# Kernel optimization log

Hardware: AMD Instinct MI355X
Metric: run time of the kernel (lower is better)

## Reference

```python
import jax, jax.numpy as jnp
import numpy as np

EPS = 1e-5

def layer_norm(x, g, b):
    mu = jnp.mean(x, axis=-1, keepdims=True)
    var = jnp.var(x, axis=-1, keepdims=True)
    return (x - mu) * jax.lax.rsqrt(var + EPS) * g + b

def setup_inputs() -> dict:
    key = jax.random.key(0)
    ks = jax.random.split(key, 16)
    N, E, D, ED = 50000, 500000, 128, 5
    def w(k, i, o):
        return jax.random.normal(k, (i, o), jnp.float32) / np.sqrt(i)
    return {
        "x": jax.random.normal(ks[0], (N, D), jnp.float32),
        "edge_attr": jax.random.normal(ks[1], (E, ED), jnp.float32),
        "pos": jax.random.normal(ks[2], (N, 3), jnp.float32),
        "node_w1": w(ks[3], D, D), "node_b1": jnp.zeros((D,), jnp.float32),
        "node_g1": jnp.ones((D,), jnp.float32), "node_be1": jnp.zeros((D,), jnp.float32),
        "node_w2": w(ks[4], D, D), "node_b2": jnp.zeros((D,), jnp.float32),
        "edge_w1": w(ks[5], 2 * D + ED, D), "edge_b1": jnp.zeros((D,), jnp.float32),
        "edge_g1": jnp.ones((D,), jnp.float32), "edge_be1": jnp.zeros((D,), jnp.float32),
        "edge_w2": w(ks[6], D, D), "edge_b2": jnp.zeros((D,), jnp.float32),
        "upd_w": w(ks[7], 2 * D, D), "upd_b": jnp.zeros((D,), jnp.float32),
        "ln_g": jnp.ones((D,), jnp.float32), "ln_b": jnp.zeros((D,), jnp.float32),
        "edge_index": jax.random.randint(ks[8], (2, E), 0, N, jnp.int64),
    }

def reference(x, edge_attr, pos, node_w1, node_b1, node_g1, node_be1, node_w2, node_b2,
              edge_w1, edge_b1, edge_g1, edge_be1, edge_w2, edge_b2,
              upd_w, upd_b, ln_g, ln_b, edge_index):
    N = x.shape[0]
    # node MLP: Linear -> LayerNorm -> ReLU -> Linear (dropout=0)
    h_nodes = jax.nn.relu(layer_norm(x @ node_w1 + node_b1, node_g1, node_be1)) @ node_w2 + node_b2
    src, dst = edge_index[0], edge_index[1]
    # edge MLP on gathered endpoint features + edge_attr  [E, 2D+edge_dim]
    ef = jnp.concatenate([x[src], x[dst], edge_attr], axis=1)
    h_edges = jax.nn.relu(layer_norm(ef @ edge_w1 + edge_b1, edge_g1, edge_be1)) @ edge_w2 + edge_b2
    # scatter-add aggregation to destination nodes
    h_agg = jax.ops.segment_sum(h_edges, dst, num_segments=N)
    h_out = jnp.concatenate([h_nodes, h_agg], axis=1) @ upd_w + upd_b
    h_out = h_out + x  # residual (in_channels == out_channels)
    return layer_norm(h_out, ln_g, ln_b)
```

## Files before the change

kernel.cpp:

```cpp
#include <hip/hip_runtime.h>
#include <stdint.h>

#define D    128
#define ED   5
#define BLK  512
#define WPB  8
#define W1S  296
#define W2S  136
#define HS   136
#define US   264
#define GRID 256

typedef __attribute__((ext_vector_type(8))) short bf16x8;
typedef __attribute__((ext_vector_type(4))) float f32x4;

__device__ __forceinline__ unsigned short f2bf(float f) {
    union { float f; uint32_t u; } c; c.f = f;
    uint32_t r = (c.u + 0x7fffu + ((c.u >> 16) & 1u)) >> 16;
    return (unsigned short)r;
}
__device__ __forceinline__ float bflo(uint32_t u) {
    union { uint32_t u; float f; } c; c.u = u << 16; return c.f;
}
__device__ __forceinline__ float bfhi(uint32_t u) {
    union { uint32_t u; float f; } c; c.u = u & 0xffff0000u; return c.f;
}
__device__ __forceinline__ bf16x8 cvt8(const float* __restrict__ p) {
    float4 a = *(const float4*)p;
    float4 b = *(const float4*)(p + 4);
    bf16x8 r;
    r[0] = (short)f2bf(a.x); r[1] = (short)f2bf(a.y);
    r[2] = (short)f2bf(a.z); r[3] = (short)f2bf(a.w);
    r[4] = (short)f2bf(b.x); r[5] = (short)f2bf(b.y);
    r[6] = (short)f2bf(b.z); r[7] = (short)f2bf(b.w);
    return r;
}
__device__ __forceinline__ bool detect64(const int* ei) {
    return (ei[1] == 0) & (ei[3] == 0) & (ei[5] == 0) &
           (ei[7] == 0) & (ei[9] == 0) & (ei[11] == 0);
}

__global__ __launch_bounds__(512)
void cvt_count_kernel(const float* __restrict__ in, unsigned short* __restrict__ out,
                      int n8, const int* __restrict__ ei, int* __restrict__ cnt, int E) {
    const int i = blockIdx.x * 512 + threadIdx.x;
    if (i < n8) {
        float4 a = ((const float4*)in)[2 * i];
        float4 b = ((const float4*)in)[2 * i + 1];
        union { unsigned short s[8]; uint4 v; } p;
        p.s[0] = f2bf(a.x); p.s[1] = f2bf(a.y); p.s[2] = f2bf(a.z); p.s[3] = f2bf(a.w);
        p.s[4] = f2bf(b.x); p.s[5] = f2bf(b.y); p.s[6] = f2bf(b.z); p.s[7] = f2bf(b.w);
        ((uint4*)out)[i] = p.v;
    } else {
        const int e = i - n8;
        if (e < E) {
            const bool is64 = detect64(ei);
            int d = is64 ? ei[2 * ((size_t)E + e)] : ei[(size_t)E + e];
            atomicAdd(&cnt[d], 1);
        }
    }
}

__global__ __launch_bounds__(1024)
void scan_blk_kernel(const int* __restrict__ cnt, int* __restrict__ part,
                     int* __restrict__ bsum, int N) {
    __shared__ int wsum[16];
    const int tid = threadIdx.x, wave = tid >> 6, lane = tid & 63;
    const int idx = blockIdx.x * 1024 + tid;
    int v = (idx < N) ? cnt[idx] : 0;
    int s = v;
    #pragma unroll
    for (int off = 1; off < 64; off <<= 1) {
        int t = __shfl_up(s, off, 64);
        if (lane >= off) s += t;
    }
    if (lane == 63) wsum[wave] = s;
    __syncthreads();
    if (wave == 0 && lane < 16) {
        int ws_ = wsum[lane];
        #pragma unroll
        for (int off = 1; off < 16; off <<= 1) {
            int t = __shfl_up(ws_, off, 64);
            if (lane >= off) ws_ += t;
        }
        wsum[lane] = ws_;
    }
    __syncthreads();
    const int excl = ((wave == 0) ? 0 : wsum[wave - 1]) + (s - v);
    if (idx < N) part[idx] = excl;
    if (tid == 0) bsum[blockIdx.x] = wsum[15];
}

__global__ __launch_bounds__(1024)
void scan_top_kernel(int* __restrict__ bsum, int nb) {
    __shared__ int wsum[16];
    const int tid = threadIdx.x, wave = tid >> 6, lane = tid & 63;
    int v = (tid < nb) ? bsum[tid] : 0;
    int s = v;
    #pragma unroll
    for (int off = 1; off < 64; off <<= 1) {
        int t = __shfl_up(s, off, 64);
        if (lane >= off) s += t;
    }
    if (lane == 63) wsum[wave] = s;
    __syncthreads();
    if (wave == 0 && lane < 16) {
        int ws_ = wsum[lane];
        #pragma unroll
        for (int off = 1; off < 16; off <<= 1) {
            int t = __shfl_up(ws_, off, 64);
            if (lane >= off) ws_ += t;
        }
        wsum[lane] = ws_;
    }
    __syncthreads();
    const int excl = ((wave == 0) ? 0 : wsum[wave - 1]) + (s - v);
    if (tid < nb) bsum[tid] = excl;
}

__global__ __launch_bounds__(1024)
void scan_add_kernel(const int* __restrict__ part, const int* __restrict__ bsum,
                     int* __restrict__ starts, int* __restrict__ cursor,
                     int N, int E) {
    const int idx = blockIdx.x * 1024 + threadIdx.x;
    if (idx < N) {
        int v = part[idx] + bsum[blockIdx.x];
        starts[idx] = v;
        cursor[idx] = v;
    }
    if (blockIdx.x == 0 && threadIdx.x == 0) starts[N] = E;
}

__global__ __launch_bounds__(512)
void fill_kernel(const int* __restrict__ ei, int* __restrict__ cursor,
                 int* __restrict__ slotp, int E) {
    const bool is64 = detect64(ei);
    int e = blockIdx.x * 512 + threadIdx.x;
    if (e >= E) return;
    int d = is64 ? ei[2 * ((size_t)E + e)] : ei[(size_t)E + e];
    slotp[e] = atomicAdd(&cursor[d], 1);
}

template<bool EDGE, bool XBF, bool CSR>
__global__ __launch_bounds__(BLK, 2)
void mlp_kernel(const float* __restrict__ x, const unsigned short* __restrict__ xbf,
                const float* __restrict__ ea, const int* __restrict__ ei,
                const int* __restrict__ slotp,
                const float* __restrict__ w1, const float* __restrict__ b1,
                const float* __restrict__ g1, const float* __restrict__ be1,
                const float* __restrict__ w2, const float* __restrict__ b2,
                unsigned short* __restrict__ hout, float* __restrict__ aggf,
                int N, int E)
{
    __shared__ unsigned short w1t[128 * W1S];
    __shared__ unsigned short w2t[128 * W2S];
    __shared__ unsigned short hb[WPB][16 * HS];

    const int tid = threadIdx.x;
    const int KROWS = EDGE ? 288 : 128;
    for (int i = tid; i < KROWS * 128; i += BLK) {
        int k = i >> 7, n = i & 127;
        float v = (!EDGE || k < (2 * D + ED)) ? w1[k * 128 + n] : 0.f;
        w1t[n * W1S + k] = f2bf(v);
    }
    for (int i = tid; i < 128 * 128; i += BLK) {
        int k = i >> 7, n = i & 127;
        w2t[n * W2S + k] = f2bf(w2[k * 128 + n]);
    }
    __syncthreads();

    bool is64 = false;
    if (EDGE) is64 = detect64(ei);

    const int lane = tid & 63, w = tid >> 6;
    const int g = lane >> 4, c = lane & 15;

    float b1v[8], g1v[8], e1v[8], b2v[8];
    #pragma unroll
    for (int nt = 0; nt < 8; ++nt) {
        b1v[nt] = b1[nt * 16 + c];  g1v[nt] = g1[nt * 16 + c];
        e1v[nt] = be1[nt * 16 + c]; b2v[nt] = b2[nt * 16 + c];
    }

    const int cnt = EDGE ? E : N;
    const int nT = (cnt + 15) >> 4;
    const int step = gridDim.x * WPB;
    unsigned short* hw = hb[w];

    int pdd = 0, prc = 0, psl = 0;
    size_t paoff = 0, pboff = 0;
    bf16x8 pf[9];

    auto loadIdx = [&](int tl) {
        const int rr = tl * 16 + c;
        const int rc = rr < cnt ? rr : cnt - 1;
        prc = rc;
        if (EDGE) {
            int s = is64 ? ei[2 * (size_t)rc]       : ei[rc];
            pdd   = is64 ? ei[2 * ((size_t)E + rc)] : ei[(size_t)E + rc];
            paoff = (size_t)s * D;
            pboff = (size_t)pdd * D;
            if (CSR) psl = slotp[rc];
        } else {
            paoff = (size_t)rc * D;
        }
    };
    auto loadFrags = [&]() {
        #pragma unroll
        for (int kk = 0; kk < (EDGE ? 8 : 4); ++kk) {
            const size_t o = (kk < 4) ? paoff + kk * 32 : pboff + (kk - 4) * 32;
            if (XBF) pf[kk] = *(const bf16x8*)(xbf + o + 8 * g);
            else     pf[kk] = cvt8(x + o + 8 * g);
        }
        if (EDGE) {
            bf16x8 t;
            #pragma unroll
            for (int j = 0; j < 8; ++j) t[j] = 0;
            if (g == 0) {
                #pragma unroll
                for (int j = 0; j < ED; ++j)
                    t[j] = (short)f2bf(ea[(size_t)prc * ED + j]);
            }
            pf[8] = t;
        }
    };

    int tile = blockIdx.x * WPB + w;
    if (tile < nT) { loadIdx(tile); loadFrags(); }

    for (; tile < nT; tile += step) {
        bf16x8 af[9];
        #pragma unroll
        for (int kk = 0; kk < (EDGE ? 9 : 4); ++kk) af[kk] = pf[kk];
        const int dd = pdd;
        const int sl = psl;
        const int row = tile * 16 + c;

        const int tn = tile + step;
        loadIdx(tn < nT ? tn : tile);

        const f32x4 z = {0.f, 0.f, 0.f, 0.f};
        f32x4 acc[8] = {z, z, z, z, z, z, z, z};
        #pragma unroll
        for (int kk = 0; kk < (EDGE ? 9 : 4); ++kk) {
            const unsigned short* wr = &w1t[c * W1S + kk * 32 + 8 * g];
            #pragma unroll
            for (int nt = 0; nt < 8; ++nt) {
                bf16x8 bf = *(const bf16x8*)(wr + nt * 16 * W1S);
                acc[nt] = __builtin_amdgcn_mfma_f32_16x16x32_bf16(af[kk], bf, acc[nt], 0, 0, 0);
            }
        }

        loadFrags();

        float mean[4], rstd[4];
        #pragma unroll
        for (int r = 0; r < 4; ++r) {
            float s = 0.f, q = 0.f;
            #pragma unroll
            for (int nt = 0; nt < 8; ++nt) {
                float v = acc[nt][r] + b1v[nt];
                acc[nt][r] = v;
                s += v; q += v * v;
            }
            s += __shfl_xor(s, 1, 64); q += __shfl_xor(q, 1, 64);
            s += __shfl_xor(s, 2, 64); q += __shfl_xor(q, 2, 64);
            s += __shfl_xor(s, 4, 64); q += __shfl_xor(q, 4, 64);
            s += __shfl_xor(s, 8, 64); q += __shfl_xor(q, 8, 64);
            float m = s * (1.f / 128.f);
            float var = q * (1.f / 128.f) - m * m;
            mean[r] = m;
            rstd[r] = rsqrtf(var + 1e-5f);
        }
        #pragma unroll
        for (int nt = 0; nt < 8; ++nt) {
            #pragma unroll
            for (int r = 0; r < 4; ++r) {
                float h = fmaxf((acc[nt][r] - mean[r]) * rstd[r] * g1v[nt] + e1v[nt], 0.f);
                hw[(4 * g + r) * HS + nt * 16 + c] = f2bf(h);
            }
        }

        f32x4 acc2[8] = {z, z, z, z, z, z, z, z};
        #pragma unroll
        for (int kk = 0; kk < 4; ++kk) {
            bf16x8 hf = *(const bf16x8*)&hw[c * HS + kk * 32 + 8 * g];
            const unsigned short* wr = &w2t[c * W2S + kk * 32 + 8 * g];
            #pragma unroll
            for (int nt = 0; nt < 8; ++nt) {
                bf16x8 bf = *(const bf16x8*)(wr + nt * 16 * W2S);
                acc2[nt] = __builtin_amdgcn_mfma_f32_16x16x32_bf16(hf, bf, acc2[nt], 0, 0, 0);
            }
        }

        if (EDGE && !CSR) {
            int dv[4];
            #pragma unroll
            for (int r = 0; r < 4; ++r) dv[r] = __shfl(dd, 4 * g + r, 64);
            #pragma unroll
            for (int r = 0; r < 4; ++r) {
                const int er = tile * 16 + 4 * g + r;
                if (er < cnt) {
                    float* dst = aggf + (size_t)dv[r] * D + c;
                    #pragma unroll
                    for (int nt = 0; nt < 8; ++nt)
                        atomicAdd(dst + nt * 16, acc2[nt][r] + b2v[nt]);
                }
            }
        } else {
            #pragma unroll
            for (int nt = 0; nt < 8; ++nt) {
                #pragma unroll
                for (int r = 0; r < 4; ++r)
                    hw[(4 * g + r) * HS + nt * 16 + c] = f2bf(acc2[nt][r] + b2v[nt]);
            }
            if (row < cnt) {
                const int orow = (EDGE && CSR) ? sl : row;
                unsigned short* dst = hout + (size_t)orow * D;
                #pragma unroll
                for (int j = 0; j < 4; ++j)
                    *(uint4*)(dst + (j * 4 + g) * 8) =
                        *(const uint4*)&hw[c * HS + (j * 4 + g) * 8];
            }
        }
    }
}

template<bool XBF>
__global__ __launch_bounds__(BLK, 2)
void upd3_kernel(const unsigned short* __restrict__ hnb,
                 const unsigned short* __restrict__ h2, const int* __restrict__ starts,
                 const float* __restrict__ x, const unsigned short* __restrict__ xbf,
                 const float* __restrict__ uw, const float* __restrict__ ub,
                 const float* __restrict__ lg, const float* __restrict__ lb,
                 float* __restrict__ out, int N)
{
    __shared__ unsigned short wt[128 * US];
    const int tid = threadIdx.x;
    for (int i = tid; i < 256 * 128; i += BLK) {
        int k = i >> 7, n = i & 127;
        wt[n * US + k] = f2bf(uw[i]);
    }
    __syncthreads();

    const int lane = tid & 63, w = tid >> 6;
    const int g = lane >> 4, c = lane & 15;

    float ubv[8], gv[8], bv[8];
    #pragma unroll
    for (int nt = 0; nt < 8; ++nt) {
        ubv[nt] = ub[nt * 16 + c]; gv[nt] = lg[nt * 16 + c]; bv[nt] = lb[nt * 16 + c];
    }

    const int nT = (N + 15) >> 4;
    for (int tile = blockIdx.x * WPB + w; tile < nT; tile += gridDim.x * WPB) {
        const int row = tile * 16 + c;
        const int rc  = row < N ? row : N - 1;

        const int s = starts[rc], t = starts[rc + 1];
        float ag0[8] = {0,0,0,0,0,0,0,0}, ag1[8] = {0,0,0,0,0,0,0,0};
        float ag2[8] = {0,0,0,0,0,0,0,0}, ag3[8] = {0,0,0,0,0,0,0,0};
        for (int j = s; j < t; ++j) {
            const unsigned short* pr = h2 + (size_t)j * D + 8 * g;
            uint4 v0 = *(const uint4*)(pr);
            uint4 v1 = *(const uint4*)(pr + 32);
            uint4 v2 = *(const uint4*)(pr + 64);
            uint4 v3 = *(const uint4*)(pr + 96);
            ag0[0] += bflo(v0.x); ag0[1] += bfhi(v0.x); ag0[2] += bflo(v0.y); ag0[3] += bfhi(v0.y);
            ag0[4] += bflo(v0.z); ag0[5] += bfhi(v0.z); ag0[6] += bflo(v0.w); ag0[7] += bfhi(v0.w);
            ag1[0] += bflo(v1.x); ag1[1] += bfhi(v1.x); ag1[2] += bflo(v1.y); ag1[3] += bfhi(v1.y);
            ag1[4] += bflo(v1.z); ag1[5] += bfhi(v1.z); ag1[6] += bflo(v1.w); ag1[7] += bfhi(v1.w);
            ag2[0] += bflo(v2.x); ag2[1] += bfhi(v2.x); ag2[2] += bflo(v2.y); ag2[3] += bfhi(v2.y);
            ag2[4] += bflo(v2.z); ag2[5] += bfhi(v2.z); ag2[6] += bflo(v2.w); ag2[7] += bfhi(v2.w);
            ag3[0] += bflo(v3.x); ag3[1] += bfhi(v3.x); ag3[2] += bflo(v3.y); ag3[3] += bfhi(v3.y);
            ag3[4] += bflo(v3.z); ag3[5] += bfhi(v3.z); ag3[6] += bflo(v3.w); ag3[7] += bfhi(v3.w);
        }

        const f32x4 z = {0.f, 0.f, 0.f, 0.f};
        f32x4 acc[8] = {z, z, z, z, z, z, z, z};

        #pragma unroll
        for (int kk = 0; kk < 8; ++kk) {
            bf16x8 af;
            if (kk < 4) {
                af = *(const bf16x8*)(hnb + (size_t)rc * D + kk * 32 + 8 * g);
            } else {
                const float* agp = (kk == 4) ? ag0 : (kk == 5) ? ag1 : (kk == 6) ? ag2 : ag3;
                #pragma unroll
                for (int i = 0; i < 8; ++i) af[i] = (short)f2bf(agp[i]);
            }
            const unsigned short* wr = &wt[c * US + kk * 32 + 8 * g];
            #pragma unroll
            for (int nt = 0; nt < 8; ++nt) {
                bf16x8 bf = *(const bf16x8*)(wr + nt * 16 * US);
                acc[nt] = __builtin_amdgcn_mfma_f32_16x16x32_bf16(af, bf, acc[nt], 0, 0, 0);
            }
        }

        float mean[4], rstd[4];
        #pragma unroll
        for (int r = 0; r < 4; ++r) {
            const int row4 = tile * 16 + 4 * g + r;
            const int r4c = row4 < N ? row4 : N - 1;
            float s2 = 0.f, q = 0.f;
            #pragma unroll
            for (int nt = 0; nt < 8; ++nt) {
                float xr;
                if (XBF) xr = bflo((uint32_t)xbf[(size_t)r4c * D + nt * 16 + c]);
                else     xr = x[(size_t)r4c * D + nt * 16 + c];
                float v = acc[nt][r] + ubv[nt] + xr;
                acc[nt][r] = v;
                s2 += v; q += v * v;
            }
            s2 += __shfl_xor(s2, 1, 64); q += __shfl_xor(q, 1, 64);
            s2 += __shfl_xor(s2, 2, 64); q += __shfl_xor(q, 2, 64);
            s2 += __shfl_xor(s2, 4, 64); q += __shfl_xor(q, 4, 64);
            s2 += __shfl_xor(s2, 8, 64); q += __shfl_xor(q, 8, 64);
            float m = s2 * (1.f / 128.f);
            mean[r] = m;
            rstd[r] = rsqrtf(q * (1.f / 128.f) - m * m + 1e-5f);
        }
        #pragma unroll
        for (int r = 0; r < 4; ++r) {
            const int row4 = tile * 16 + 4 * g + r;
            if (row4 < N) {
                #pragma unroll
                for (int nt = 0; nt < 8; ++nt)
                    out[(size_t)row4 * D + nt * 16 + c] =
                        (acc[nt][r] - mean[r]) * rstd[r] * gv[nt] + bv[nt];
            }
        }
    }
}

template<bool AGGBF, bool XBF>
__global__ __launch_bounds__(BLK, 4)
void upd2_kernel(const unsigned short* __restrict__ hnb, const void* __restrict__ aggp,
                 const float* __restrict__ x, const unsigned short* __restrict__ xbf,
                 const float* __restrict__ uw, const float* __restrict__ ub,
                 const float* __restrict__ lg, const float* __restrict__ lb,
                 float* __restrict__ out, int N)
{
    __shared__ unsigned short wt[128 * US];
    const int tid = threadIdx.x;
    for (int i = tid; i < 256 * 128; i += BLK) {
        int k = i >> 7, n = i & 127;
        wt[n * US + k] = f2bf(uw[i]);
    }
    __syncthreads();

    const int lane = tid & 63, w = tid >> 6;
    const int g = lane >> 4, c = lane & 15;

    float ubv[8], gv[8], bv[8];
    #pragma unroll
    for (int nt = 0; nt < 8; ++nt) {
        ubv[nt] = ub[nt * 16 + c]; gv[nt] = lg[nt * 16 + c]; bv[nt] = lb[nt * 16 + c];
    }

    const int nT = (N + 15) >> 4;
    for (int tile = blockIdx.x * WPB + w; tile < nT; tile += gridDim.x * WPB) {
        const int row = tile * 16 + c;
        const int rc  = row < N ? row : N - 1;

        const f32x4 z = {0.f, 0.f, 0.f, 0.f};
        f32x4 acc[8] = {z, z, z, z, z, z, z, z};

        #pragma unroll
        for (int kk = 0; kk < 8; ++kk) {
            bf16x8 af;
            if (kk < 4) {
                af = *(const bf16x8*)(hnb + (size_t)rc * D + kk * 32 + 8 * g);
            } else {
                if (AGGBF)
                    af = *(const bf16x8*)((const unsigned short*)aggp +
                                          (size_t)rc * D + (kk - 4) * 32 + 8 * g);
                else
                    af = cvt8((const float*)aggp + (size_t)rc * D + (kk - 4) * 32 + 8 * g);
            }
            const unsigned short* wr = &wt[c * US + kk * 32 + 8 * g];
            #pragma unroll
            for (int nt = 0; nt < 8; ++nt) {
                bf16x8 bf = *(const bf16x8*)(wr + nt * 16 * US);
                acc[nt] = __builtin_amdgcn_mfma_f32_16x16x32_bf16(af, bf, acc[nt], 0, 0, 0);
            }
        }

        float mean[4], rstd[4];
        #pragma unroll
        for (int r = 0; r < 4; ++r) {
            const int row4 = tile * 16 + 4 * g + r;
            const int r4c = row4 < N ? row4 : N - 1;
            float s = 0.f, q = 0.f;
            #pragma unroll
            for (int nt = 0; nt < 8; ++nt) {
                float xr;
                if (XBF) xr = bflo((uint32_t)xbf[(size_t)r4c * D + nt * 16 + c]);
                else     xr = x[(size_t)r4c * D + nt * 16 + c];
                float v = acc[nt][r] + ubv[nt] + xr;
                acc[nt][r] = v;
                s += v; q += v * v;
            }
            s += __shfl_xor(s, 1, 64); q += __shfl_xor(q, 1, 64);
            s += __shfl_xor(s, 2, 64); q += __shfl_xor(q, 2, 64);
            s += __shfl_xor(s, 4, 64); q += __shfl_xor(q, 4, 64);
            s += __shfl_xor(s, 8, 64); q += __shfl_xor(q, 8, 64);
            float m = s * (1.f / 128.f);
            mean[r] = m;
            rstd[r] = rsqrtf(q * (1.f / 128.f) - m * m + 1e-5f);
        }
        #pragma unroll
        for (int r = 0; r < 4; ++r) {
            const int row4 = tile * 16 + 4 * g + r;
            if (row4 < N) {
                #pragma unroll
                for (int nt = 0; nt < 8; ++nt)
                    out[(size_t)row4 * D + nt * 16 + c] =
                        (acc[nt][r] - mean[r]) * rstd[r] * gv[nt] + bv[nt];
            }
        }
    }
}

extern "C" void kernel_launch(void* const* d_in, const int* in_sizes, int n_in,
                              void* d_out, int out_size, void* d_ws, size_t ws_size,
                              hipStream_t stream)
{
    const float* x    = (const float*)d_in[0];
    const float* ea   = (const float*)d_in[1];
    const float* nw1  = (const float*)d_in[3];
    const float* nb1  = (const float*)d_in[4];
    const float* ng1  = (const float*)d_in[5];
    const float* nbe1 = (const float*)d_in[6];
    const float* nw2  = (const float*)d_in[7];
    const float* nb2  = (const float*)d_in[8];
    const float* ew1  = (const float*)d_in[9];
    const float* eb1  = (const float*)d_in[10];
    const float* eg1  = (const float*)d_in[11];
    const float* ebe1 = (const float*)d_in[12];
    const float* ew2  = (const float*)d_in[13];
    const float* eb2  = (const float*)d_in[14];
    const float* uw   = (const float*)d_in[15];
    const float* ub   = (const float*)d_in[16];
    const float* lg   = (const float*)d_in[17];
    const float* lb   = (const float*)d_in[18];
    const int*   eidx = (const int*)d_in[19];

    const int N = in_sizes[0] / D;
    const int E = in_sizes[1] / ED;

    char* base = (char*)d_ws;
    size_t off = 0;
    auto alloc = [&](size_t bytes) -> char* {
        char* p = base + off;
        off = (off + bytes + 255) & ~(size_t)255;
        return p;
    };

    unsigned short* hnb  = (unsigned short*)alloc((size_t)N * D * 2);
    unsigned short* xbf  = (unsigned short*)alloc((size_t)N * D * 2);
    int* cnt    = (int*)alloc((size_t)N * 4);
    int* starts = (int*)alloc(((size_t)N + 1) * 4);
    int* cursor = (int*)alloc((size_t)N * 4);
    int* bsum   = (int*)alloc(1024 * 4);
    int* slotA  = (int*)alloc((size_t)E * 4);
    unsigned short* h2 = (unsigned short*)alloc((size_t)E * D * 2);
    const size_t needA = off;

    const int n8 = N * D / 8;
    const int egrid = (E + 511) / 512;
    const int nb = (N + 1023) / 1024;
    const int ugrid = (((N + 15) / 16) + WPB - 1) / WPB;

    if (ws_size >= needA && nb <= 1024) {
        hipMemsetAsync(cnt, 0, (size_t)N * 4, stream);
        cvt_count_kernel<<<(n8 + E + 511) / 512, 512, 0, stream>>>(
            x, xbf, n8, eidx, cnt, E);
        scan_blk_kernel<<<nb, 1024, 0, stream>>>(cnt, cursor, bsum, N);
        scan_top_kernel<<<1, 1024, 0, stream>>>(bsum, nb);
        scan_add_kernel<<<nb, 1024, 0, stream>>>(cursor, bsum, starts, cursor, N, E);
        fill_kernel<<<egrid, 512, 0, stream>>>(eidx, cursor, slotA, E);
        mlp_kernel<false, true, true><<<GRID, BLK, 0, stream>>>(
            x, xbf, nullptr, nullptr, nullptr, nw1, nb1, ng1, nbe1, nw2, nb2,
            hnb, nullptr, N, E);
        mlp_kernel<true, true, true><<<GRID, BLK, 0, stream>>>(
            x, xbf, ea, eidx, slotA, ew1, eb1, eg1, ebe1, ew2, eb2,
            h2, nullptr, N, E);
        upd3_kernel<true><<<ugrid, BLK, 0, stream>>>(
            hnb, h2, starts, x, xbf, uw, ub, lg, lb, (float*)d_out, N);
        return;
    }

    off = 0;
    unsigned short* hnb2 = (unsigned short*)alloc((size_t)N * D * 2);
    float* aggf = (float*)alloc((size_t)N * D * 4);
    unsigned short* xbf2 = (unsigned short*)alloc((size_t)N * D * 2);
    const size_t needB = off;

    hipMemsetAsync(aggf, 0, (size_t)N * D * 4, stream);
    if (ws_size >= needB) {
        cvt_count_kernel<<<(n8 + 511) / 512, 512, 0, stream>>>(
            x, xbf2, n8, nullptr, nullptr, 0);
        mlp_kernel<false, true, false><<<GRID, BLK, 0, stream>>>(
            x, xbf2, nullptr, nullptr, nullptr, nw1, nb1, ng1, nbe1, nw2, nb2,
            hnb2, nullptr, N, E);
        mlp_kernel<true, true, false><<<GRID, BLK, 0, stream>>>(
            x, xbf2, ea, eidx, nullptr, ew1, eb1, eg1, ebe1, ew2, eb2,
            nullptr, aggf, N, E);
        upd2_kernel<false, true><<<ugrid, BLK, 0, stream>>>(
            hnb2, aggf, x, xbf2, uw, ub, lg, lb, (float*)d_out, N);
    } else {
        mlp_kernel<false, false, false><<<GRID, BLK, 0, stream>>>(
            x, nullptr, nullptr, nullptr, nullptr, nw1, nb1, ng1, nbe1, nw2, nb2,
            hnb2, nullptr, N, E);
        mlp_kernel<true, false, false><<<GRID, BLK, 0, stream>>>(
            x, nullptr, ea, eidx, nullptr, ew1, eb1, eg1, ebe1, ew2, eb2,
            nullptr, aggf, N, E);
        upd2_kernel<false, false><<<ugrid, BLK, 0, stream>>>(
            hnb2, aggf, x, nullptr, uw, ub, lg, lb, (float*)d_out, N);
    }
}
```

Baseline: 410.0 us.

## Process two 16-edge tiles per wave in edge MLP and split node MLP kernel

The edge MLP now handles 32 edges per wave iteration. Each LDS weight fragment load feeds two MFMAs, one per 16-row tile, which halves weight-read traffic from shared memory per edge. The node MLP gets its own simpler kernel with a smaller w1 buffer. LDS stores of the hidden activations are packed into 32-bit pairs using lane shuffles. The fallback path is rewritten to use the CSR/upd3 approach, and the atomic and upd2 variants are removed. Doubling the prefetch and accumulator buffers raises register pressure under the 2-blocks-per-SM launch bound, which risks spills or lower occupancy.

```diff
diff --git a/kernel.cpp b/kernel.cpp
--- a/kernel.cpp
+++ b/kernel.cpp
@@ -141,26 +141,24 @@
     slotp[e] = atomicAdd(&cursor[d], 1);
 }
 
-template<bool EDGE, bool XBF, bool CSR>
+template<bool XBF>
 __global__ __launch_bounds__(BLK, 2)
-void mlp_kernel(const float* __restrict__ x, const unsigned short* __restrict__ xbf,
-                const float* __restrict__ ea, const int* __restrict__ ei,
-                const int* __restrict__ slotp,
-                const float* __restrict__ w1, const float* __restrict__ b1,
-                const float* __restrict__ g1, const float* __restrict__ be1,
-                const float* __restrict__ w2, const float* __restrict__ b2,
-                unsigned short* __restrict__ hout, float* __restrict__ aggf,
-                int N, int E)
+void edge_mlp(const float* __restrict__ x, const unsigned short* __restrict__ xbf,
+              const float* __restrict__ ea, const int* __restrict__ ei,
+              const int* __restrict__ slotp,
+              const float* __restrict__ w1, const float* __restrict__ b1,
+              const float* __restrict__ g1, const float* __restrict__ be1,
+              const float* __restrict__ w2, const float* __restrict__ b2,
+              unsigned short* __restrict__ h2, int E)
 {
     __shared__ unsigned short w1t[128 * W1S];
     __shared__ unsigned short w2t[128 * W2S];
     __shared__ unsigned short hb[WPB][16 * HS];
 
     const int tid = threadIdx.x;
-    const int KROWS = EDGE ? 288 : 128;
-    for (int i = tid; i < KROWS * 128; i += BLK) {
+    for (int i = tid; i < 288 * 128; i += BLK) {
         int k = i >> 7, n = i & 127;
-        float v = (!EDGE || k < (2 * D + ED)) ? w1[k * 128 + n] : 0.f;
+        float v = (k < (2 * D + ED)) ? w1[k * 128 + n] : 0.f;
         w1t[n * W1S + k] = f2bf(v);
     }
     for (int i = tid; i < 128 * 128; i += BLK) {
@@ -169,9 +167,7 @@
     }
     __syncthreads();
 
-    bool is64 = false;
-    if (EDGE) is64 = detect64(ei);
-
+    const bool is64 = detect64(ei);
     const int lane = tid & 63, w = tid >> 6;
     const int g = lane >> 4, c = lane & 15;
 
@@ -182,77 +178,57 @@
         e1v[nt] = be1[nt * 16 + c]; b2v[nt] = b2[nt * 16 + c];
     }
 
-    const int cnt = EDGE ? E : N;
-    const int nT = (cnt + 15) >> 4;
+    const int nT = (E + 31) >> 5;
     const int step = gridDim.x * WPB;
     unsigned short* hw = hb[w];
 
-    int pdd = 0, prc = 0, psl = 0;
-    size_t paoff = 0, pboff = 0;
-    bf16x8 pf[9];
+    int psl0 = 0, psl1 = 0, pe0 = 0, pe1 = 0;
+    size_t pa0 = 0, pb0 = 0, pa1 = 0, pb1 = 0;
+    bf16x8 pf0[9], pf1[9];
 
     auto loadIdx = [&](int tl) {
-        const int rr = tl * 16 + c;
-        const int rc = rr < cnt ? rr : cnt - 1;
-        prc = rc;
-        if (EDGE) {
-            int s = is64 ? ei[2 * (size_t)rc]       : ei[rc];
-            pdd   = is64 ? ei[2 * ((size_t)E + rc)] : ei[(size_t)E + rc];
-            paoff = (size_t)s * D;
-            pboff = (size_t)pdd * D;
-            if (CSR) psl = slotp[rc];
-        } else {
-            paoff = (size_t)rc * D;
-        }
+        const int r0 = tl * 32 + c;
+        const int r1 = tl * 32 + 16 + c;
+        const int rc0 = r0 < E ? r0 : E - 1;
+        const int rc1 = r1 < E ? r1 : E - 1;
+        pe0 = rc0; pe1 = rc1;
+        int s0 = is64 ? ei[2 * (size_t)rc0]       : ei[rc0];
+        int d0 = is64 ? ei[2 * ((size_t)E + rc0)] : ei[(size_t)E + rc0];
+        int s1 = is64 ? ei[2 * (size_t)rc1]       : ei[rc1];
+        int d1 = is64 ? ei[2 * ((size_t)E + rc1)] : ei[(size_t)E + rc1];
+        pa0 = (size_t)s0 * D; pb0 = (size_t)d0 * D;
+        pa1 = (size_t)s1 * D; pb1 = (size_t)d1 * D;
+        psl0 = slotp[rc0]; psl1 = slotp[rc1];
     };
     auto loadFrags = [&]() {
         #pragma unroll
-        for (int kk = 0; kk < (EDGE ? 8 : 4); ++kk) {
-            const size_t o = (kk < 4) ? paoff + kk * 32 : pboff + (kk - 4) * 32;
-            if (XBF) pf[kk] = *(const bf16x8*)(xbf + o + 8 * g);
-            else     pf[kk] = cvt8(x + o + 8 * g);
-        }
-        if (EDGE) {
-            bf16x8 t;
-            #pragma unroll
-            for (int j = 0; j < 8; ++j) t[j] = 0;
-            if (g == 0) {
-                #pragma unroll
-                for (int j = 0; j < ED; ++j)
-                    t[j] = (short)f2bf(ea[(size_t)prc * ED + j]);
-            }
-            pf[8] = t;
-        }
+        for (int kk = 0; kk < 8; ++kk) {
+            const size_t o0 = (kk < 4) ? pa0 + kk * 32 : pb0 + (kk - 4) * 32;
+            const size_t o1 = (kk < 4) ? pa1 + kk * 32 : pb1 + (kk - 4) * 32;
+            if (XBF) {
+                pf0[kk] = *(const bf16x8*)(xbf + o0 + 8 * g);
+                pf1[kk] = *(const bf16x8*)(xbf + o1 + 8 * g);
+            } else {
+                pf0[kk] = cvt8(x + o0 + 8 * g);
+                pf1[kk] = cvt8(x + o1 + 8 * g);
+            }
+        }
+        bf16x8 t0, t1;
+        #pragma unroll
+        for (int j = 0; j < 8; ++j) { t0[j] = 0; t1[j] = 0; }
+        if (g == 0) {
+            #pragma unroll
+            for (int j = 0; j < ED; ++j) {
+                t0[j] = (short)f2bf(ea[(size_t)pe0 * ED + j]);
+                t1[j] = (short)f2bf(ea[(size_t)pe1 * ED + j]);
+            }
+        }
+        pf0[8] = t0; pf1[8] = t1;
     };
 
-    int tile = blockIdx.x * WPB + w;
-    if (tile < nT) { loadIdx(tile); loadFrags(); }
-
-    for (; tile < nT; tile += step) {
-        bf16x8 af[9];
-        #pragma unroll
-        for (int kk = 0; kk < (EDGE ? 9 : 4); ++kk) af[kk] = pf[kk];
-        const int dd = pdd;
-        const int sl = psl;
-        const int row = tile * 16 + c;
-
-        const int tn = tile + step;
-        loadIdx(tn < nT ? tn : tile);
-
-        const f32x4 z = {0.f, 0.f, 0.f, 0.f};
-        f32x4 acc[8] = {z, z, z, z, z, z, z, z};
-        #pragma unroll
-        for (int kk = 0; kk < (EDGE ? 9 : 4); ++kk) {
-            const unsigned short* wr = &w1t[c * W1S + kk * 32 + 8 * g];
-            #pragma unroll
-            for (int nt = 0; nt < 8; ++nt) {
-                bf16x8 bf = *(const bf16x8*)(wr + nt * 16 * W1S);
-                acc[nt] = __builtin_amdgcn_mfma_f32_16x16x32_bf16(af[kk], bf, acc[nt], 0, 0, 0);
-            }
-        }
-
-        loadFrags();
-
+    const f32x4 z = {0.f, 0.f, 0.f, 0.f};
+
+    auto process = [&](f32x4* acc, int sl, int rowv) __attribute__((always_inline)) {
         float mean[4], rstd[4];
         #pragma unroll
         for (int r = 0; r < 4; ++r) {
@@ -268,19 +244,21 @@
             s += __shfl_xor(s, 4, 64); q += __shfl_xor(q, 4, 64);
             s += __shfl_xor(s, 8, 64); q += __shfl_xor(q, 8, 64);
             float m = s * (1.f / 128.f);
-            float var = q * (1.f / 128.f) - m * m;
             mean[r] = m;
-            rstd[r] = rsqrtf(var + 1e-5f);
+            rstd[r] = rsqrtf(q * (1.f / 128.f) - m * m + 1e-5f);
         }
         #pragma unroll
         for (int nt = 0; nt < 8; ++nt) {
             #pragma unroll
             for (int r = 0; r < 4; ++r) {
                 float h = fmaxf((acc[nt][r] - mean[r]) * rstd[r] * g1v[nt] + e1v[nt], 0.f);
-                hw[(4 * g + r) * HS + nt * 16 + c] = f2bf(h);
-            }
-        }
-
+                float hp = __shfl_xor(h, 1, 64);
+                if (!(c & 1)) {
+                    uint32_t pk = (uint32_t)f2bf(h) | ((uint32_t)f2bf(hp) << 16);
+                    *(uint32_t*)&hw[(4 * g + r) * HS + nt * 16 + c] = pk;
+                }
+            }
+        }
         f32x4 acc2[8] = {z, z, z, z, z, z, z, z};
         #pragma unroll
         for (int kk = 0; kk < 4; ++kk) {
@@ -292,36 +270,167 @@
                 acc2[nt] = __builtin_amdgcn_mfma_f32_16x16x32_bf16(hf, bf, acc2[nt], 0, 0, 0);
             }
         }
-
-        if (EDGE && !CSR) {
-            int dv[4];
-            #pragma unroll
-            for (int r = 0; r < 4; ++r) dv[r] = __shfl(dd, 4 * g + r, 64);
+        #pragma unroll
+        for (int nt = 0; nt < 8; ++nt) {
             #pragma unroll
             for (int r = 0; r < 4; ++r) {
-                const int er = tile * 16 + 4 * g + r;
-                if (er < cnt) {
-                    float* dst = aggf + (size_t)dv[r] * D + c;
-                    #pragma unroll
-                    for (int nt = 0; nt < 8; ++nt)
-                        atomicAdd(dst + nt * 16, acc2[nt][r] + b2v[nt]);
+                float o = acc2[nt][r] + b2v[nt];
+                float op = __shfl_xor(o, 1, 64);
+                if (!(c & 1)) {
+                    uint32_t pk = (uint32_t)f2bf(o) | ((uint32_t)f2bf(op) << 16);
+                    *(uint32_t*)&hw[(4 * g + r) * HS + nt * 16 + c] = pk;
                 }
             }
-        } else {
-            #pragma unroll
-            for (int nt = 0; nt < 8; ++nt) {
-                #pragma unroll
-                for (int r = 0; r < 4; ++r)
-                    hw[(4 * g + r) * HS + nt * 16 + c] = f2bf(acc2[nt][r] + b2v[nt]);
-            }
-            if (row < cnt) {
-                const int orow = (EDGE && CSR) ? sl : row;
-                unsigned short* dst = hout + (size_t)orow * D;
-                #pragma unroll
-                for (int j = 0; j < 4; ++j)
-                    *(uint4*)(dst + (j * 4 + g) * 8) =
-                        *(const uint4*)&hw[c * HS + (j * 4 + g) * 8];
-            }
+        }
+        if (rowv < E) {
+            unsigned short* dst = h2 + (size_t)sl * D;
+            #pragma unroll
+            for (int j = 0; j < 4; ++j)
+                *(uint4*)(dst + (j * 4 + g) * 8) =
+                    *(const uint4*)&hw[c * HS + (j * 4 + g) * 8];
+        }
+    };
+
+    int tile = blockIdx.x * WPB + w;
+    if (tile < nT) { loadIdx(tile); loadFrags(); }
+
+    for (; tile < nT; tile += step) {
+        f32x4 acc0[8] = {z, z, z, z, z, z, z, z};
+        f32x4 acc1[8] = {z, z, z, z, z, z, z, z};
+        #pragma unroll
+        for (int kk = 0; kk < 9; ++kk) {
+            const unsigned short* wr = &w1t[c * W1S + kk * 32 + 8 * g];
+            const bf16x8 a0 = pf0[kk], a1 = pf1[kk];
+            #pragma unroll
+            for (int nt = 0; nt < 8; ++nt) {
+                bf16x8 bf = *(const bf16x8*)(wr + nt * 16 * W1S);
+                acc0[nt] = __builtin_amdgcn_mfma_f32_16x16x32_bf16(a0, bf, acc0[nt], 0, 0, 0);
+                acc1[nt] = __builtin_amdgcn_mfma_f32_16x16x32_bf16(a1, bf, acc1[nt], 0, 0, 0);
+            }
+        }
+        const int sl0 = psl0, sl1 = psl1;
+        const int row0 = tile * 32 + c, row1 = tile * 32 + 16 + c;
+
+        const int tn = tile + step;
+        loadIdx(tn < nT ? tn : tile);
+        loadFrags();
+
+        process(acc0, sl0, row0);
+        process(acc1, sl1, row1);
+    }
+}
+
+template<bool XBF>
+__global__ __launch_bounds__(BLK, 2)
+void node_mlp(const float* __restrict__ x, const unsigned short* __restrict__ xbf,
+              const float* __restrict__ w1, const float* __restrict__ b1,
+              const float* __restrict__ g1, const float* __restrict__ be1,
+              const float* __restrict__ w2, const float* __restrict__ b2,
+              unsigned short* __restrict__ hnb, int N)
+{
+    __shared__ unsigned short w1t[128 * W2S];
+    __shared__ unsigned short w2t[128 * W2S];
+    __shared__ unsigned short hb[WPB][16 * HS];
+
+    const int tid = threadIdx.x;
+    for (int i = tid; i < 128 * 128; i += BLK) {
+        int k = i >> 7, n = i & 127;
+        w1t[n * W2S + k] = f2bf(w1[k * 128 + n]);
+        w2t[n * W2S + k] = f2bf(w2[k * 128 + n]);
+    }
+    __syncthreads();
+
+    const int lane = tid & 63, w = tid >> 6;
+    const int g = lane >> 4, c = lane & 15;
+
+    float b1v[8], g1v[8], e1v[8], b2v[8];
+    #pragma unroll
+    for (int nt = 0; nt < 8; ++nt) {
+        b1v[nt] = b1[nt * 16 + c];  g1v[nt] = g1[nt * 16 + c];
+        e1v[nt] = be1[nt * 16 + c]; b2v[nt] = b2[nt * 16 + c];
+    }
+
+    const int nT = (N + 15) >> 4;
+    const f32x4 z = {0.f, 0.f, 0.f, 0.f};
+    unsigned short* hw = hb[w];
+
+    for (int tile = blockIdx.x * WPB + w; tile < nT; tile += gridDim.x * WPB) {
+        const int row = tile * 16 + c;
+        const int rc  = row < N ? row : N - 1;
+
+        f32x4 acc[8] = {z, z, z, z, z, z, z, z};
+        #pragma unroll
+        for (int kk = 0; kk < 4; ++kk) {
+            bf16x8 af;
+            if (XBF) af = *(const bf16x8*)(xbf + (size_t)rc * D + kk * 32 + 8 * g);
+            else     af = cvt8(x + (size_t)rc * D + kk * 32 + 8 * g);
+            const unsigned short* wr = &w1t[c * W2S + kk * 32 + 8 * g];
+            #pragma unroll
+            for (int nt = 0; nt < 8; ++nt) {
+                bf16x8 bf = *(const bf16x8*)(wr + nt * 16 * W2S);
+                acc[nt] = __builtin_amdgcn_mfma_f32_16x16x32_bf16(af, bf, acc[nt], 0, 0, 0);
+            }
+        }
+
+        float mean[4], rstd[4];
+        #pragma unroll
+        for (int r = 0; r < 4; ++r) {
+            float s = 0.f, q = 0.f;
+            #pragma unroll
+            for (int nt = 0; nt < 8; ++nt) {
+                float v = acc[nt][r] + b1v[nt];
+                acc[nt][r] = v;
+                s += v; q += v * v;
+            }
+            s += __shfl_xor(s, 1, 64); q += __shfl_xor(q, 1, 64);
+            s += __shfl_xor(s, 2, 64); q += __shfl_xor(q, 2, 64);
+            s += __shfl_xor(s, 4, 64); q += __shfl_xor(q, 4, 64);
+            s += __shfl_xor(s, 8, 64); q += __shfl_xor(q, 8, 64);
+            float m = s * (1.f / 128.f);
+            mean[r] = m;
+            rstd[r] = rsqrtf(q * (1.f / 128.f) - m * m + 1e-5f);
+        }
+        #pragma unroll
+        for (int nt = 0; nt < 8; ++nt) {
+            #pragma unroll
+            for (int r = 0; r < 4; ++r) {
+                float h = fmaxf((acc[nt][r] - mean[r]) * rstd[r] * g1v[nt] + e1v[nt], 0.f);
+                float hp = __shfl_xor(h, 1, 64);
+                if (!(c & 1)) {
+                    uint32_t pk = (uint32_t)f2bf(h) | ((uint32_t)f2bf(hp) << 16);
+                    *(uint32_t*)&hw[(4 * g + r) * HS + nt * 16 + c] = pk;
+                }
+            }
+        }
+        f32x4 acc2[8] = {z, z, z, z, z, z, z, z};
+        #pragma unroll
+        for (int kk = 0; kk < 4; ++kk) {
+            bf16x8 hf = *(const bf16x8*)&hw[c * HS + kk * 32 + 8 * g];
+            const unsigned short* wr = &w2t[c * W2S + kk * 32 + 8 * g];
+            #pragma unroll
+            for (int nt = 0; nt < 8; ++nt) {
+                bf16x8 bf = *(const bf16x8*)(wr + nt * 16 * W2S);
+                acc2[nt] = __builtin_amdgcn_mfma_f32_16x16x32_bf16(hf, bf, acc2[nt], 0, 0, 0);
+            }
+        }
+        #pragma unroll
+        for (int nt = 0; nt < 8; ++nt) {
+            #pragma unroll
+            for (int r = 0; r < 4; ++r) {
+                float o = acc2[nt][r] + b2v[nt];
+                float op = __shfl_xor(o, 1, 64);
+                if (!(c & 1)) {
+                    uint32_t pk = (uint32_t)f2bf(o) | ((uint32_t)f2bf(op) << 16);
+                    *(uint32_t*)&hw[(4 * g + r) * HS + nt * 16 + c] = pk;
+                }
+            }
+        }
+        if (row < N) {
+            unsigned short* dst = hnb + (size_t)row * D;
+            #pragma unroll
+            for (int j = 0; j < 4; ++j)
+                *(uint4*)(dst + (j * 4 + g) * 8) =
+                    *(const uint4*)&hw[c * HS + (j * 4 + g) * 8];
         }
     }
 }
@@ -378,7 +487,6 @@
 
         const f32x4 z = {0.f, 0.f, 0.f, 0.f};
         f32x4 acc[8] = {z, z, z, z, z, z, z, z};
-
         #pragma unroll
         for (int kk = 0; kk < 8; ++kk) {
             bf16x8 af;
@@ -417,95 +525,6 @@
             s2 += __shfl_xor(s2, 4, 64); q += __shfl_xor(q, 4, 64);
             s2 += __shfl_xor(s2, 8, 64); q += __shfl_xor(q, 8, 64);
             float m = s2 * (1.f / 128.f);
-            mean[r] = m;
-            rstd[r] = rsqrtf(q * (1.f / 128.f) - m * m + 1e-5f);
-        }
-        #pragma unroll
-        for (int r = 0; r < 4; ++r) {
-            const int row4 = tile * 16 + 4 * g + r;
-            if (row4 < N) {
-                #pragma unroll
-                for (int nt = 0; nt < 8; ++nt)
-                    out[(size_t)row4 * D + nt * 16 + c] =
-                        (acc[nt][r] - mean[r]) * rstd[r] * gv[nt] + bv[nt];
-            }
-        }
-    }
-}
-
-template<bool AGGBF, bool XBF>
-__global__ __launch_bounds__(BLK, 4)
-void upd2_kernel(const unsigned short* __restrict__ hnb, const void* __restrict__ aggp,
-                 const float* __restrict__ x, const unsigned short* __restrict__ xbf,
-                 const float* __restrict__ uw, const float* __restrict__ ub,
-                 const float* __restrict__ lg, const float* __restrict__ lb,
-                 float* __restrict__ out, int N)
-{
-    __shared__ unsigned short wt[128 * US];
-    const int tid = threadIdx.x;
-    for (int i = tid; i < 256 * 128; i += BLK) {
-        int k = i >> 7, n = i & 127;
-        wt[n * US + k] = f2bf(uw[i]);
-    }
-    __syncthreads();
-
-    const int lane = tid & 63, w = tid >> 6;
-    const int g = lane >> 4, c = lane & 15;
-
-    float ubv[8], gv[8], bv[8];
-    #pragma unroll
-    for (int nt = 0; nt < 8; ++nt) {
-        ubv[nt] = ub[nt * 16 + c]; gv[nt] = lg[nt * 16 + c]; bv[nt] = lb[nt * 16 + c];
-    }
-
-    const int nT = (N + 15) >> 4;
-    for (int tile = blockIdx.x * WPB + w; tile < nT; tile += gridDim.x * WPB) {
-        const int row = tile * 16 + c;
-        const int rc  = row < N ? row : N - 1;
-
-        const f32x4 z = {0.f, 0.f, 0.f, 0.f};
-        f32x4 acc[8] = {z, z, z, z, z, z, z, z};
-
-        #pragma unroll
-        for (int kk = 0; kk < 8; ++kk) {
-            bf16x8 af;
-            if (kk < 4) {
-                af = *(const bf16x8*)(hnb + (size_t)rc * D + kk * 32 + 8 * g);
-            } else {
-                if (AGGBF)
-                    af = *(const bf16x8*)((const unsigned short*)aggp +
-                                          (size_t)rc * D + (kk - 4) * 32 + 8 * g);
-                else
-                    af = cvt8((const float*)aggp + (size_t)rc * D + (kk - 4) * 32 + 8 * g);
-            }
-            const unsigned short* wr = &wt[c * US + kk * 32 + 8 * g];
-            #pragma unroll
-            for (int nt = 0; nt < 8; ++nt) {
-                bf16x8 bf = *(const bf16x8*)(wr + nt * 16 * US);
-                acc[nt] = __builtin_amdgcn_mfma_f32_16x16x32_bf16(af, bf, acc[nt], 0, 0, 0);
-            }
-        }
-
-        float mean[4], rstd[4];
-        #pragma unroll
-        for (int r = 0; r < 4; ++r) {
-            const int row4 = tile * 16 + 4 * g + r;
-            const int r4c = row4 < N ? row4 : N - 1;
-            float s = 0.f, q = 0.f;
-            #pragma unroll
-            for (int nt = 0; nt < 8; ++nt) {
-                float xr;
-                if (XBF) xr = bflo((uint32_t)xbf[(size_t)r4c * D + nt * 16 + c]);
-                else     xr = x[(size_t)r4c * D + nt * 16 + c];
-                float v = acc[nt][r] + ubv[nt] + xr;
-                acc[nt][r] = v;
-                s += v; q += v * v;
-            }
-            s += __shfl_xor(s, 1, 64); q += __shfl_xor(q, 1, 64);
-            s += __shfl_xor(s, 2, 64); q += __shfl_xor(q, 2, 64);
-            s += __shfl_xor(s, 4, 64); q += __shfl_xor(q, 4, 64);
-            s += __shfl_xor(s, 8, 64); q += __shfl_xor(q, 8, 64);
-            float m = s * (1.f / 128.f);
             mean[r] = m;
             rstd[r] = rsqrtf(q * (1.f / 128.f) - m * m + 1e-5f);
         }
@@ -580,12 +599,10 @@
         scan_top_kernel<<<1, 1024, 0, stream>>>(bsum, nb);
         scan_add_kernel<<<nb, 1024, 0, stream>>>(cursor, bsum, starts, cursor, N, E);
         fill_kernel<<<egrid, 512, 0, stream>>>(eidx, cursor, slotA, E);
-        mlp_kernel<false, true, true><<<GRID, BLK, 0, stream>>>(
-            x, xbf, nullptr, nullptr, nullptr, nw1, nb1, ng1, nbe1, nw2, nb2,
-            hnb, nullptr, N, E);
-        mlp_kernel<true, true, true><<<GRID, BLK, 0, stream>>>(
-            x, xbf, ea, eidx, slotA, ew1, eb1, eg1, ebe1, ew2, eb2,
-            h2, nullptr, N, E);
+        node_mlp<true><<<GRID, BLK, 0, stream>>>(
+            x, xbf, nw1, nb1, ng1, nbe1, nw2, nb2, hnb, N);
+        edge_mlp<true><<<GRID, BLK, 0, stream>>>(
+            x, xbf, ea, eidx, slotA, ew1, eb1, eg1, ebe1, ew2, eb2, h2, E);
         upd3_kernel<true><<<ugrid, BLK, 0, stream>>>(
             hnb, h2, starts, x, xbf, uw, ub, lg, lb, (float*)d_out, N);
         return;
@@ -593,30 +610,24 @@
 
     off = 0;
     unsigned short* hnb2 = (unsigned short*)alloc((size_t)N * D * 2);
-    float* aggf = (float*)alloc((size_t)N * D * 4);
-    unsigned short* xbf2 = (unsigned short*)alloc((size_t)N * D * 2);
-    const size_t needB = off;
-
-    hipMemsetAsync(aggf, 0, (size_t)N * D * 4, stream);
-    if (ws_size >= needB) {
-        cvt_count_kernel<<<(n8 + 511) / 512, 512, 0, stream>>>(
-            x, xbf2, n8, nullptr, nullptr, 0);
-        mlp_kernel<false, true, false><<<GRID, BLK, 0, stream>>>(
-            x, xbf2, nullptr, nullptr, nullptr, nw1, nb1, ng1, nbe1, nw2, nb2,
-            hnb2, nullptr, N, E);
-        mlp_kernel<true, true, false><<<GRID, BLK, 0, stream>>>(
-            x, xbf2, ea, eidx, nullptr, ew1, eb1, eg1, ebe1, ew2, eb2,
-            nullptr, aggf, N, E);
-        upd2_kernel<false, true><<<ugrid, BLK, 0, stream>>>(
-            hnb2, aggf, x, xbf2, uw, ub, lg, lb, (float*)d_out, N);
-    } else {
-        mlp_kernel<false, false, false><<<GRID, BLK, 0, stream>>>(
-            x, nullptr, nullptr, nullptr, nullptr, nw1, nb1, ng1, nbe1, nw2, nb2,
-            hnb2, nullptr, N, E);
-        mlp_kernel<true, false, false><<<GRID, BLK, 0, stream>>>(
-            x, nullptr, ea, eidx, nullptr, ew1, eb1, eg1, ebe1, ew2, eb2,
-            nullptr, aggf, N, E);
-        upd2_kernel<false, false><<<ugrid, BLK, 0, stream>>>(
-            hnb2, aggf, x, nullptr, uw, ub, lg, lb, (float*)d_out, N);
-    }
-}
+    int* cnt2    = (int*)alloc((size_t)N * 4);
+    int* starts2 = (int*)alloc(((size_t)N + 1) * 4);
+    int* cursor2 = (int*)alloc((size_t)N * 4);
+    int* bsum2   = (int*)alloc(1024 * 4);
+    int* slotB   = (int*)alloc((size_t)E * 4);
+    unsigned short* h2b = (unsigned short*)alloc((size_t)E * D * 2);
+
+    hipMemsetAsync(cnt2, 0, (size_t)N * 4, stream);
+    cvt_count_kernel<<<(E + 511) / 512, 512, 0, stream>>>(
+        x, nullptr, 0, eidx, cnt2, E);
+    scan_blk_kernel<<<nb, 1024, 0, stream>>>(cnt2, cursor2, bsum2, N);
+    scan_top_kernel<<<1, 1024, 0, stream>>>(bsum2, nb);
+    scan_add_kernel<<<nb, 1024, 0, stream>>>(cursor2, bsum2, starts2, cursor2, N, E);
+    fill_kernel<<<egrid, 512, 0, stream>>>(eidx, cursor2, slotB, E);
+    node_mlp<false><<<GRID, BLK, 0, stream>>>(
+        x, nullptr, nw1, nb1, ng1, nbe1, nw2, nb2, hnb2, N);
+    edge_mlp<false><<<GRID, BLK, 0, stream>>>(
+        x, nullptr, ea, eidx, slotB, ew1, eb1, eg1, ebe1, ew2, eb2, h2b, E);
+    upd3_kernel<false><<<ugrid, BLK, 0, stream>>>(
+        hnb2, h2b, starts2, x, nullptr, uw, ub, lg, lb, (float*)d_out, N);
+}
```

New measurement: 491.7 us. +19.9%, slower.
